# Kernel tuning notes

Measured on AMD Instinct MI355X. Metric: run time of the kernel, lower is better.

## Reference

```python
import jax, jax.numpy as jnp
import numpy as np

NUM_CLASSES = 32
TRI = NUM_CLASSES * (NUM_CLASSES - 1) // 2      # 496 class pairs
HID = 32 * TRI                                  # 15872 total hidden
IN = 512
B = 256
RATIO = 0.0

# pair -> (i, j) class indices, in the same enumeration order as the torch idx formula
_I_IDX, _J_IDX = np.triu_indices(NUM_CLASSES, k=1)
_I_IDX = jnp.asarray(_I_IDX)
_J_IDX = jnp.asarray(_J_IDX)


def setup_inputs() -> dict:
    key = jax.random.key(0)
    ks = jax.random.split(key, 7)
    s = 0.02  # small init so activations stay sane
    return {
        "x": jax.random.normal(ks[0], (B, IN), jnp.float32),
        "W1": jax.random.normal(ks[1], (IN, HID), jnp.float32) * s,
        "b1": jax.random.normal(ks[2], (HID,), jnp.float32) * s,
        "W2": jax.random.normal(ks[3], (HID, HID), jnp.float32) * s,
        "b2": jax.random.normal(ks[4], (HID,), jnp.float32) * s,
        "Wout": jax.random.normal(ks[5], (HID, 2 * TRI), jnp.float32) * s,
        "bout": jax.random.normal(ks[6], (2 * TRI,), jnp.float32) * s,
    }


def reference(x, W1, b1, W2, b2, Wout, bout):
    # MLP stack: fc1 + relu, fc2 + relu (num_layers=2), fc_out
    h = jax.nn.relu(x @ W1 + b1)                 # [B, HID]
    h = jax.nn.relu(h @ W2 + b2)                 # [B, HID]
    out = h @ Wout + bout                        # [B, 2*TRI]

    # vote scatter: out[:, 2p], out[:, 2p+1] are the (i, j) logits of pair p
    pair = out.reshape(B, TRI, 2)                # [B, TRI, 2]
    d = pair[..., 0] - pair[..., 1]              # [B, TRI]
    # original condition: d > ratio  OR  -d >= ratio   (always true at ratio=0)
    mask = (d > RATIO) | (-d >= RATIO)
    vi = jnp.where(mask, pair[..., 0], 0.0)      # contribution to class i
    vj = jnp.where(mask, pair[..., 1], 0.0)      # contribution to class j

    votes = jnp.zeros((B, NUM_CLASSES), jnp.float32)
    votes = votes.at[:, _I_IDX].add(vi)
    votes = votes.at[:, _J_IDX].add(vj)
    return votes
```

## Files before the change

kernel.cpp:

```cpp
#include <hip/hip_runtime.h>

using short8 = __attribute__((ext_vector_type(8))) short;
using f32x16 = __attribute__((ext_vector_type(16))) float;
using f32x4  = __attribute__((ext_vector_type(4))) float;
using us4    = __attribute__((ext_vector_type(4))) unsigned short;

#define NHID 15872

__device__ __forceinline__ unsigned short f2bf(float f) {
  unsigned u = __builtin_bit_cast(unsigned, f);
  u += 0x7fff + ((u >> 16) & 1);
  return (unsigned short)(u >> 16);
}
__device__ __forceinline__ float bf2f(unsigned short h) {
  return __builtin_bit_cast(float, ((unsigned)h) << 16);
}
__device__ __forceinline__ int swz(int col, int c) {
  return (c ^ (col & 7) ^ ((col >> 3) & 7)) & 7;
}

__global__ void cvt_x(const float* __restrict__ x, unsigned short* __restrict__ xb) {
  int i = (blockIdx.x * 256 + threadIdx.x) * 4;
  float4 v = *reinterpret_cast<const float4*>(x + i);
  us4 o;
  o[0] = f2bf(v.x); o[1] = f2bf(v.y); o[2] = f2bf(v.z); o[3] = f2bf(v.w);
  *reinterpret_cast<us4*>(xb + i) = o;
}


#define LOADB(R, T) do { _Pragma("unroll") \
  for (int r_ = 0; r_ < 4; ++r_) \
    R[r_] = *reinterpret_cast<const f32x4*>(bbase + ((size_t)(T) * 64 + r_) * NHID); \
} while (0)

#define CVTW(R, BUF) do { _Pragma("unroll") \
  for (int c2_ = 0; c2_ < 4; ++c2_) { \
    int col_ = cq * 4 + c2_; \
    int wa_ = col_ * 64 + swz(col_, kst >> 1) * 8 + (kst & 1) * 4; \
    us4 o_; \
    _Pragma("unroll") \
    for (int r_ = 0; r_ < 4; ++r_) o_[r_] = f2bf(R[r_][c2_]); \
    *reinterpret_cast<us4*>(&Blds[BUF][wa_]) = o_; \
  } \
} while (0)

#define MFMAP(BUF, T) do { \
  const unsigned short* at_ = abase + (size_t)(T) * 64; \
  short8 a_[4]; \
  _Pragma("unroll") \
  for (int ks_ = 0; ks_ < 4; ++ks_) \
    a_[ks_] = *reinterpret_cast<const short8*>(at_ + ks_ * 16); \
  _Pragma("unroll") \
  for (int ks_ = 0; ks_ < 4; ++ks_) { \
    int c_ = ks_ * 2 + hi; \
    short8 b0_ = *reinterpret_cast<const short8*>(&Blds[BUF][(l31) * 64 + swz(l31, c_) * 8]); \
    short8 b1_ = *reinterpret_cast<const short8*>(&Blds[BUF][(32 + l31) * 64 + swz(32 + l31, c_) * 8]); \
    short8 b2_ = *reinterpret_cast<const short8*>(&Blds[BUF][(64 + l31) * 64 + swz(64 + l31, c_) * 8]); \
    short8 b3_ = *reinterpret_cast<const short8*>(&Blds[BUF][(96 + l31) * 64 + swz(96 + l31, c_) * 8]); \
    acc0 = __builtin_amdgcn_mfma_f32_32x32x16_bf16(a_[ks_], b0_, acc0, 0, 0, 0); \
    acc1 = __builtin_amdgcn_mfma_f32_32x32x16_bf16(a_[ks_], b1_, acc1, 0, 0, 0); \
    acc2 = __builtin_amdgcn_mfma_f32_32x32x16_bf16(a_[ks_], b2_, acc2, 0, 0, 0); \
    acc3 = __builtin_amdgcn_mfma_f32_32x32x16_bf16(a_[ks_], b3_, acc3, 0, 0, 0); \
  } \
} while (0)

template<bool FINAL>
__global__ __launch_bounds__(512, 4)
void gemm_v5(const unsigned short* __restrict__ A, int lda, int KC,
             const float* __restrict__ B, const float* __restrict__ bias,
             unsigned short* __restrict__ Cf, float* __restrict__ Cp)
{
  __shared__ short Blds[2][128 * 64];
  const int tid  = threadIdx.x;
  const int n0   = blockIdx.x * 128;
  const int ks0  = blockIdx.y;
  const int k0   = ks0 * KC;
  const int lane = tid & 63;
  const int w    = tid >> 6;
  const int l31  = lane & 31;
  const int hi   = lane >> 5;

  f32x16 acc0 = {}, acc1 = {}, acc2 = {}, acc3 = {};

  const int cq  = tid & 31;
  const int kst = tid >> 5;
  const float* bbase = B + (size_t)(k0 + kst * 4) * NHID + n0 + cq * 4;
  const unsigned short* abase = A + (size_t)(w * 32 + l31) * lda + k0 + hi * 8;

  f32x4 rA[4], rB[4];
  const int NT = KC >> 6;

  LOADB(rA, 0);
  LOADB(rB, 1);
  CVTW(rA, 0);
  __syncthreads();

  for (int t = 0; t < NT - 2; t += 2) {
    LOADB(rA, t + 2);
    MFMAP(0, t);
    CVTW(rB, 1);
    __syncthreads();
    LOADB(rB, t + 3);
    MFMAP(1, t + 1);
    CVTW(rA, 0);
    __syncthreads();
  }
  MFMAP(0, NT - 2);
  CVTW(rB, 1);
  __syncthreads();
  MFMAP(1, NT - 1);

#define STOREC(ACC, CBLK) do { \
    int col_ = n0 + (CBLK) * 32 + l31; \
    if (FINAL) { \
      float bv_ = bias[col_]; \
      _Pragma("unroll") \
      for (int reg_ = 0; reg_ < 16; ++reg_) { \
        int row_ = w * 32 + (reg_ & 3) + 8 * (reg_ >> 2) + 4 * hi; \
        float v_ = ACC[reg_] + bv_; v_ = v_ > 0.f ? v_ : 0.f; \
        Cf[(size_t)row_ * NHID + col_] = f2bf(v_); \
      } \
    } else { \
      float* base_ = Cp + (size_t)ks0 * 256 * NHID; \
      _Pragma("unroll") \
      for (int reg_ = 0; reg_ < 16; ++reg_) { \
        int row_ = w * 32 + (reg_ & 3) + 8 * (reg_ >> 2) + 4 * hi; \
        base_[(size_t)row_ * NHID + col_] = ACC[reg_]; \
      } \
    } \
  } while (0)

  STOREC(acc0, 0);
  STOREC(acc1, 1);
  STOREC(acc2, 2);
  STOREC(acc3, 3);
#undef STOREC
}

__global__ void reduce_h2(const float* __restrict__ part, const float* __restrict__ bias,
                          unsigned short* __restrict__ h2, int S) {
  size_t g = ((size_t)blockIdx.x * 256 + threadIdx.x) * 4;
  int c = (int)(g % NHID);
  float4 s = *reinterpret_cast<const float4*>(part + g);
  for (int k = 1; k < S; ++k) {
    float4 p = *reinterpret_cast<const float4*>(part + (size_t)k * 256 * NHID + g);
    s.x += p.x; s.y += p.y; s.z += p.z; s.w += p.w;
  }
  float4 b = *reinterpret_cast<const float4*>(bias + c);
  s.x += b.x; s.y += b.y; s.z += b.z; s.w += b.w;
  us4 o;
  o[0] = f2bf(s.x > 0.f ? s.x : 0.f);
  o[1] = f2bf(s.y > 0.f ? s.y : 0.f);
  o[2] = f2bf(s.z > 0.f ? s.z : 0.f);
  o[3] = f2bf(s.w > 0.f ? s.w : 0.f);
  *reinterpret_cast<us4*>(h2 + g) = o;
}

__global__ void wv_fold(const float* __restrict__ Wout, float* __restrict__ Wv) {
  int g = blockIdx.x * 256 + threadIdx.x;
  int k = g >> 5, c = g & 31;
  const float* row = Wout + (size_t)k * 992;
  float s = 0.f;
#pragma unroll
  for (int o = 0; o < 32; ++o) {
    if (o == c) continue;
    int i = c < o ? c : o;
    int j = c < o ? o : c;
    int p = 31 * i - (i * (i - 1)) / 2 + (j - i - 1);
    s += row[2 * p + (c > o ? 1 : 0)];
  }
  Wv[g] = s;
}

__global__ void votes_partial(const unsigned short* __restrict__ h2,
                              const float* __restrict__ Wv,
                              float* __restrict__ part) {
  int bm = blockIdx.x >> 5;
  int ks = blockIdx.x & 31;
  int r  = bm * 8 + (threadIdx.x >> 5);
  int c  = threadIdx.x & 31;
  const unsigned short* hrow = h2 + (size_t)r * NHID + ks * 496;
  const float* wp = Wv + (size_t)(ks * 496) * 32 + c;
  float s = 0.f;
  for (int k0 = 0; k0 < 496; k0 += 8) {
    short8 hv = *reinterpret_cast<const short8*>(hrow + k0);
#pragma unroll
    for (int j = 0; j < 8; ++j)
      s += bf2f((unsigned short)hv[j]) * wp[(size_t)(k0 + j) * 32];
  }
  part[(size_t)(ks * 256 + r) * 32 + c] = s;
}

__global__ void votes_reduce(const float* __restrict__ part,
                             const float* __restrict__ bout,
                             float* __restrict__ out) {
  int g = blockIdx.x * 256 + threadIdx.x;
  int c = g & 31;
  float s = 0.f;
#pragma unroll
  for (int ks = 0; ks < 32; ++ks) s += part[(size_t)ks * 8192 + g];
  float bv = 0.f;
#pragma unroll
  for (int o = 0; o < 32; ++o) {
    if (o == c) continue;
    int i = c < o ? c : o;
    int j = c < o ? o : c;
    int p = 31 * i - (i * (i - 1)) / 2 + (j - i - 1);
    bv += bout[2 * p + (c > o ? 1 : 0)];
  }
  out[g] = s + bv;
}

extern "C" void kernel_launch(void* const* d_in, const int* in_sizes, int n_in,
                              void* d_out, int out_size, void* d_ws, size_t ws_size,
                              hipStream_t stream) {
  const float* x    = (const float*)d_in[0];
  const float* W1   = (const float*)d_in[1];
  const float* b1   = (const float*)d_in[2];
  const float* W2   = (const float*)d_in[3];
  const float* b2   = (const float*)d_in[4];
  const float* Wout = (const float*)d_in[5];
  const float* bout = (const float*)d_in[6];
  float* out = (float*)d_out;

  char* ws = (char*)d_ws;
  unsigned short* xb = (unsigned short*)(ws);
  unsigned short* h1 = (unsigned short*)(ws + 262144);
  unsigned short* h2 = (unsigned short*)(ws + 8388608);
  float*          Wv = (float*)(ws + 16515072);
  float*        part = (float*)(ws + 18546688);
  float*       part2 = (float*)(ws + 19595264);

  const size_t PART1 = (size_t)256 * NHID * 4;
  int S = 1;
  if (ws_size >= 19595264ull + 4 * PART1) S = 4;
  else if (ws_size >= 19595264ull + 2 * PART1) S = 2;

  hipLaunchKernelGGL(cvt_x, dim3(128), dim3(256), 0, stream, x, xb);
  hipLaunchKernelGGL((gemm_v5<true>), dim3(124, 1), dim3(512), 0, stream,
                     xb, 512, 512, W1, b1, h1, (float*)nullptr);
  if (S > 1) {
    hipLaunchKernelGGL((gemm_v5<false>), dim3(124, S), dim3(512), 0, stream,
                       h1, NHID, NHID / S, W2, (const float*)nullptr,
                       (unsigned short*)nullptr, part2);
    hipLaunchKernelGGL(reduce_h2, dim3(3968), dim3(256), 0, stream, part2, b2, h2, S);
  } else {
    hipLaunchKernelGGL((gemm_v5<true>), dim3(124, 1), dim3(512), 0, stream,
                       h1, NHID, NHID, W2, b2, h2, (float*)nullptr);
  }
  hipLaunchKernelGGL(wv_fold,       dim3(1984), dim3(256), 0, stream, Wout, Wv);
  hipLaunchKernelGGL(votes_partial, dim3(1024), dim3(256), 0, stream, h2, Wv, part);
  hipLaunchKernelGGL(votes_reduce,  dim3(32),   dim3(256), 0, stream, part, bout, out);
}
```

Before: 457.0 us.

## Replace LDS-staged GEMM with direct register B loads and swizzled split-K grid

The GEMM kernel stops staging fp32 weights through shared memory. Each lane now loads its own B fragment straight from global memory, converts it to bf16 with the hardware conversion intrinsic, and feeds the MFMA. Blocks shrink to 256 threads on 64-column tiles, and the split-K launch becomes a 1D grid whose block index is swizzled so that neighbouring blocks share K-slices. The aim is to remove LDS writes, barriers and swizzle overhead from what is a weight-bandwidth-bound GEMM. The cost is scalar, strided global loads (one float per lane per row), which may coalesce worse and raise register pressure.

```diff
diff --git a/kernel.cpp b/kernel.cpp
--- a/kernel.cpp
+++ b/kernel.cpp
@@ -1,8 +1,8 @@
 #include <hip/hip_runtime.h>
+#include <hip/hip_bf16.h>
 
 using short8 = __attribute__((ext_vector_type(8))) short;
 using f32x16 = __attribute__((ext_vector_type(16))) float;
-using f32x4  = __attribute__((ext_vector_type(4))) float;
 using us4    = __attribute__((ext_vector_type(4))) unsigned short;
 
 #define NHID 15872
@@ -12,11 +12,12 @@
   u += 0x7fff + ((u >> 16) & 1);
   return (unsigned short)(u >> 16);
 }
+__device__ __forceinline__ short f2bf_hw(float f) {
+  __hip_bfloat16 h = __float2bfloat16(f);
+  return __builtin_bit_cast(short, h);
+}
 __device__ __forceinline__ float bf2f(unsigned short h) {
   return __builtin_bit_cast(float, ((unsigned)h) << 16);
-}
-__device__ __forceinline__ int swz(int col, int c) {
-  return (c ^ (col & 7) ^ ((col >> 3) & 7)) & 7;
 }
 
 __global__ void cvt_x(const float* __restrict__ x, unsigned short* __restrict__ xb) {
@@ -28,95 +29,84 @@
 }
 
 
-#define LOADB(R, T) do { _Pragma("unroll") \
-  for (int r_ = 0; r_ < 4; ++r_) \
-    R[r_] = *reinterpret_cast<const f32x4*>(bbase + ((size_t)(T) * 64 + r_) * NHID); \
-} while (0)
-
-#define CVTW(R, BUF) do { _Pragma("unroll") \
-  for (int c2_ = 0; c2_ < 4; ++c2_) { \
-    int col_ = cq * 4 + c2_; \
-    int wa_ = col_ * 64 + swz(col_, kst >> 1) * 8 + (kst & 1) * 4; \
-    us4 o_; \
+#define LOADB16(R, S) do { \
+    const float* bp_ = bbase + (size_t)(S) * 16 * NHID; \
     _Pragma("unroll") \
-    for (int r_ = 0; r_ < 4; ++r_) o_[r_] = f2bf(R[r_][c2_]); \
-    *reinterpret_cast<us4*>(&Blds[BUF][wa_]) = o_; \
-  } \
-} while (0)
-
-#define MFMAP(BUF, T) do { \
-  const unsigned short* at_ = abase + (size_t)(T) * 64; \
-  short8 a_[4]; \
-  _Pragma("unroll") \
-  for (int ks_ = 0; ks_ < 4; ++ks_) \
-    a_[ks_] = *reinterpret_cast<const short8*>(at_ + ks_ * 16); \
-  _Pragma("unroll") \
-  for (int ks_ = 0; ks_ < 4; ++ks_) { \
-    int c_ = ks_ * 2 + hi; \
-    short8 b0_ = *reinterpret_cast<const short8*>(&Blds[BUF][(l31) * 64 + swz(l31, c_) * 8]); \
-    short8 b1_ = *reinterpret_cast<const short8*>(&Blds[BUF][(32 + l31) * 64 + swz(32 + l31, c_) * 8]); \
-    short8 b2_ = *reinterpret_cast<const short8*>(&Blds[BUF][(64 + l31) * 64 + swz(64 + l31, c_) * 8]); \
-    short8 b3_ = *reinterpret_cast<const short8*>(&Blds[BUF][(96 + l31) * 64 + swz(96 + l31, c_) * 8]); \
-    acc0 = __builtin_amdgcn_mfma_f32_32x32x16_bf16(a_[ks_], b0_, acc0, 0, 0, 0); \
-    acc1 = __builtin_amdgcn_mfma_f32_32x32x16_bf16(a_[ks_], b1_, acc1, 0, 0, 0); \
-    acc2 = __builtin_amdgcn_mfma_f32_32x32x16_bf16(a_[ks_], b2_, acc2, 0, 0, 0); \
-    acc3 = __builtin_amdgcn_mfma_f32_32x32x16_bf16(a_[ks_], b3_, acc3, 0, 0, 0); \
-  } \
-} while (0)
-
-template<bool FINAL>
-__global__ __launch_bounds__(512, 4)
-void gemm_v5(const unsigned short* __restrict__ A, int lda, int KC,
+    for (int nb_ = 0; nb_ < 2; ++nb_) { \
+      _Pragma("unroll") \
+      for (int j_ = 0; j_ < 8; ++j_) \
+        R[nb_ * 8 + j_] = bp_[(size_t)j_ * NHID + nb_ * 32]; \
+    } \
+  } while (0)
+
+#define LOADA(S) do { \
+    const unsigned short* ap_ = abase + (size_t)(S) * 16; \
+    a0 = *reinterpret_cast<const short8*>(ap_); \
+    a1 = *reinterpret_cast<const short8*>(ap_ + (size_t)32 * lda); \
+  } while (0)
+
+#define STEPM(R) do { \
+    short8 b0_, b1_; \
+    _Pragma("unroll") \
+    for (int j_ = 0; j_ < 8; ++j_) { \
+      b0_[j_] = f2bf_hw(R[j_]); \
+      b1_[j_] = f2bf_hw(R[8 + j_]); \
+    } \
+    acc0 = __builtin_amdgcn_mfma_f32_32x32x16_bf16(a0, b0_, acc0, 0, 0, 0); \
+    acc1 = __builtin_amdgcn_mfma_f32_32x32x16_bf16(a0, b1_, acc1, 0, 0, 0); \
+    acc2 = __builtin_amdgcn_mfma_f32_32x32x16_bf16(a1, b0_, acc2, 0, 0, 0); \
+    acc3 = __builtin_amdgcn_mfma_f32_32x32x16_bf16(a1, b1_, acc3, 0, 0, 0); \
+  } while (0)
+
+template<bool FINAL, bool SWZ>
+__global__ __launch_bounds__(256, 4)
+void gemm_v6(const unsigned short* __restrict__ A, int lda, int KC,
              const float* __restrict__ B, const float* __restrict__ bias,
              unsigned short* __restrict__ Cf, float* __restrict__ Cp)
 {
-  __shared__ short Blds[2][128 * 64];
+  int nidx, ks0;
+  if (SWZ) {
+    int w_ = blockIdx.x;
+    ks0  = (w_ & 7) >> 1;
+    nidx = ((w_ >> 3) << 1) | (w_ & 1);
+  } else {
+    ks0 = blockIdx.y; nidx = blockIdx.x;
+  }
+  const int n0 = nidx * 64;
+  const int k0 = ks0 * KC;
   const int tid  = threadIdx.x;
-  const int n0   = blockIdx.x * 128;
-  const int ks0  = blockIdx.y;
-  const int k0   = ks0 * KC;
+  const int w    = tid >> 6;
   const int lane = tid & 63;
-  const int w    = tid >> 6;
   const int l31  = lane & 31;
   const int hi   = lane >> 5;
+  const int m0   = w * 64;
 
   f32x16 acc0 = {}, acc1 = {}, acc2 = {}, acc3 = {};
 
-  const int cq  = tid & 31;
-  const int kst = tid >> 5;
-  const float* bbase = B + (size_t)(k0 + kst * 4) * NHID + n0 + cq * 4;
-  const unsigned short* abase = A + (size_t)(w * 32 + l31) * lda + k0 + hi * 8;
-
-  f32x4 rA[4], rB[4];
-  const int NT = KC >> 6;
-
-  LOADB(rA, 0);
-  LOADB(rB, 1);
-  CVTW(rA, 0);
-  __syncthreads();
-
-  for (int t = 0; t < NT - 2; t += 2) {
-    LOADB(rA, t + 2);
-    MFMAP(0, t);
-    CVTW(rB, 1);
-    __syncthreads();
-    LOADB(rB, t + 3);
-    MFMAP(1, t + 1);
-    CVTW(rA, 0);
-    __syncthreads();
-  }
-  MFMAP(0, NT - 2);
-  CVTW(rB, 1);
-  __syncthreads();
-  MFMAP(1, NT - 1);
-
-#define STOREC(ACC, CBLK) do { \
-    int col_ = n0 + (CBLK) * 32 + l31; \
+  const unsigned short* abase = A + (size_t)(m0 + l31) * lda + k0 + hi * 8;
+  const float* bbase = B + (size_t)(k0 + hi * 8) * NHID + n0 + l31;
+
+  const int NK = KC >> 4;
+  float bfA[16], bfB[16];
+  short8 a0, a1;
+
+  LOADB16(bfA, 0);
+  for (int s = 0; s + 2 <= NK; s += 2) {
+    LOADA(s);
+    LOADB16(bfB, s + 1);
+    STEPM(bfA);
+    LOADA(s + 1);
+    if (s + 2 < NK) LOADB16(bfA, s + 2);
+    STEPM(bfB);
+  }
+
+#define STOREC(ACC, MB, NB) do { \
+    int col_ = n0 + (NB) * 32 + l31; \
     if (FINAL) { \
       float bv_ = bias[col_]; \
       _Pragma("unroll") \
       for (int reg_ = 0; reg_ < 16; ++reg_) { \
-        int row_ = w * 32 + (reg_ & 3) + 8 * (reg_ >> 2) + 4 * hi; \
+        int row_ = m0 + (MB) * 32 + (reg_ & 3) + 8 * (reg_ >> 2) + 4 * hi; \
         float v_ = ACC[reg_] + bv_; v_ = v_ > 0.f ? v_ : 0.f; \
         Cf[(size_t)row_ * NHID + col_] = f2bf(v_); \
       } \
@@ -124,16 +114,16 @@
       float* base_ = Cp + (size_t)ks0 * 256 * NHID; \
       _Pragma("unroll") \
       for (int reg_ = 0; reg_ < 16; ++reg_) { \
-        int row_ = w * 32 + (reg_ & 3) + 8 * (reg_ >> 2) + 4 * hi; \
+        int row_ = m0 + (MB) * 32 + (reg_ & 3) + 8 * (reg_ >> 2) + 4 * hi; \
         base_[(size_t)row_ * NHID + col_] = ACC[reg_]; \
       } \
     } \
   } while (0)
 
-  STOREC(acc0, 0);
-  STOREC(acc1, 1);
-  STOREC(acc2, 2);
-  STOREC(acc3, 3);
+  STOREC(acc0, 0, 0);
+  STOREC(acc1, 0, 1);
+  STOREC(acc2, 1, 0);
+  STOREC(acc3, 1, 1);
 #undef STOREC
 }
 
@@ -232,20 +222,18 @@
   float*       part2 = (float*)(ws + 19595264);
 
   const size_t PART1 = (size_t)256 * NHID * 4;
-  int S = 1;
-  if (ws_size >= 19595264ull + 4 * PART1) S = 4;
-  else if (ws_size >= 19595264ull + 2 * PART1) S = 2;
+  const bool split4 = ws_size >= 19595264ull + 4 * PART1;
 
   hipLaunchKernelGGL(cvt_x, dim3(128), dim3(256), 0, stream, x, xb);
-  hipLaunchKernelGGL((gemm_v5<true>), dim3(124, 1), dim3(512), 0, stream,
+  hipLaunchKernelGGL((gemm_v6<true, false>), dim3(248, 1), dim3(256), 0, stream,
                      xb, 512, 512, W1, b1, h1, (float*)nullptr);
-  if (S > 1) {
-    hipLaunchKernelGGL((gemm_v5<false>), dim3(124, S), dim3(512), 0, stream,
-                       h1, NHID, NHID / S, W2, (const float*)nullptr,
+  if (split4) {
+    hipLaunchKernelGGL((gemm_v6<false, true>), dim3(992), dim3(256), 0, stream,
+                       h1, NHID, NHID / 4, W2, (const float*)nullptr,
                        (unsigned short*)nullptr, part2);
-    hipLaunchKernelGGL(reduce_h2, dim3(3968), dim3(256), 0, stream, part2, b2, h2, S);
+    hipLaunchKernelGGL(reduce_h2, dim3(3968), dim3(256), 0, stream, part2, b2, h2, 4);
   } else {
-    hipLaunchKernelGGL((gemm_v5<true>), dim3(124, 1), dim3(512), 0, stream,
+    hipLaunchKernelGGL((gemm_v6<true, false>), dim3(248, 1), dim3(256), 0, stream,
                        h1, NHID, NHID, W2, b2, h2, (float*)nullptr);
   }
   hipLaunchKernelGGL(wv_fold,       dim3(1984), dim3(256), 0, stream, Wout, Wv);
```

Measured after the change: 854.0 us. +86.9%, slower.
